# Kernel optimization log

Measured on AMD Instinct MI355X. Metric: run time of the kernel, lower is better.

## Reference

```python
import jax, jax.numpy as jnp
import numpy as np
import math

HIDDEN = 128

def setup_inputs() -> dict:
    key = jax.random.key(0)
    k1, k2, k3 = jax.random.split(key, 3)
    X = jax.random.normal(k1, (4, 4096, HIDDEN), dtype=jnp.float32)
    # nn.Linear(hidden, 3*hidden): weight [3H, H], bias [3H]
    bound = 1.0 / math.sqrt(HIDDEN)
    W = jax.random.uniform(k2, (3 * HIDDEN, HIDDEN), minval=-bound, maxval=bound, dtype=jnp.float32)
    b = jax.random.uniform(k3, (3 * HIDDEN,), minval=-bound, maxval=bound, dtype=jnp.float32)
    return {"X": X, "W": W, "b": b}

def reference(X, W, b):
    H = X.shape[-1]
    # fused QKV projection: X @ W^T + b -> [B, S, 3H]
    qkv = jnp.einsum('bsh,oh->bso', X, W) + b
    Q, K, V = jnp.split(qkv, 3, axis=-1)
    # scaled dot-product attention (single head)
    scores = jnp.einsum('bqh,bkh->bqk', Q, K) / jnp.sqrt(jnp.asarray(H, X.dtype))
    weights = jax.nn.softmax(scores, axis=-1)
    return jnp.einsum('bqk,bkh->bqh', weights, V)
```

## Files before the change

### kernel.cpp

```cpp
#include <hip/hip_runtime.h>
#include <hip/hip_fp16.h>

typedef _Float16 f16;
typedef __attribute__((ext_vector_type(8))) _Float16 f16x8;
typedef __attribute__((ext_vector_type(4))) float f32x4;
typedef __attribute__((ext_vector_type(4))) unsigned int u32x4;
typedef __attribute__((ext_vector_type(2))) unsigned int u32x2;

#define BB 4
#define SS 4096
#define HH 128
#define SC2 0.12752462157076558f
#define M2  5.7707801635558535f

union H2U { __half2 h; unsigned int u; };
union VU { u32x4 v; unsigned short s[8]; };
union F8U { u32x4 u; f16x8 h; };

__global__ __launch_bounds__(256) void wcvt(const float* __restrict__ W,
                                            f16* __restrict__ Wh)
{
    const int idx = (blockIdx.x * 256 + threadIdx.x) * 4;
    float4 v = *(const float4*)(W + idx);
    H2U h0, h1;
    h0.h = __floats2half2_rn(v.x, v.y);
    h1.h = __floats2half2_rn(v.z, v.w);
    u32x2 pk; pk.x = h0.u; pk.y = h1.u;
    *(u32x2*)(Wh + idx) = pk;
}

__global__ __launch_bounds__(256, 2) void qkv_gemm(
    const float* __restrict__ X, const f16* __restrict__ Wh,
    const float* __restrict__ bias, f16* __restrict__ Qh,
    f16* __restrict__ Kh, f16* __restrict__ Vh)
{
    const int bid = blockIdx.x;
    const int t = threadIdx.x;
    const int w = t >> 6, lane = t & 63;
    const int c = lane & 15, quad = lane >> 4;
    const int rbase = bid * 64;

    f16x8 wf[6][4];
#pragma unroll
    for (int mt = 0; mt < 6; ++mt) {
        const f16* wr = Wh + (size_t)(w * 96 + mt * 16 + c) * HH + quad * 8;
#pragma unroll
        for (int kc = 0; kc < 4; ++kc)
            wf[mt][kc] = *(const f16x8*)(wr + kc * 32);
    }
    float4 bb[6];
#pragma unroll
    for (int mt = 0; mt < 6; ++mt)
        bb[mt] = *(const float4*)&bias[w * 96 + mt * 16 + quad * 4];

#pragma unroll
    for (int nt = 0; nt < 4; ++nt) {
        f16x8 xf[4];
        const float* xr = X + (size_t)(rbase + nt * 16 + c) * HH + quad * 8;
#pragma unroll
        for (int kc = 0; kc < 4; ++kc) {
            float4 a = *(const float4*)(xr + kc * 32);
            float4 b = *(const float4*)(xr + kc * 32 + 4);
            H2U u0, u1, u2, u3;
            u0.h = __floats2half2_rn(a.x, a.y);
            u1.h = __floats2half2_rn(a.z, a.w);
            u2.h = __floats2half2_rn(b.x, b.y);
            u3.h = __floats2half2_rn(b.z, b.w);
            F8U pk; pk.u.x = u0.u; pk.u.y = u1.u; pk.u.z = u2.u; pk.u.w = u3.u;
            xf[kc] = pk.h;
        }
        f32x4 acc[6];
#pragma unroll
        for (int mt = 0; mt < 6; ++mt) acc[mt] = (f32x4)0.f;
#pragma unroll
        for (int kc = 0; kc < 4; ++kc)
#pragma unroll
            for (int mt = 0; mt < 6; ++mt)
                acc[mt] = __builtin_amdgcn_mfma_f32_16x16x32_f16(wf[mt][kc], xf[kc], acc[mt], 0, 0, 0);

        const int xrow = rbase + nt * 16 + c;
#pragma unroll
        for (int mt = 0; mt < 6; ++mt) {
            const int gcol = w * 96 + mt * 16;
            const int seg = gcol >> 7;
            const int cc = (gcol & 127) + quad * 4;
            f16* dst = (seg == 0) ? Qh : (seg == 1) ? Kh : Vh;
            H2U h0, h1;
            h0.h = __floats2half2_rn(acc[mt][0] + bb[mt].x, acc[mt][1] + bb[mt].y);
            h1.h = __floats2half2_rn(acc[mt][2] + bb[mt].z, acc[mt][3] + bb[mt].w);
            u32x2 pk; pk.x = h0.u; pk.y = h1.u;
            *(u32x2*)(dst + (size_t)xrow * HH + cc) = pk;
        }
    }
}

#define BM 128
#define BN 64
#define LK 136
#define LV 72
#define LP 40

__global__ __launch_bounds__(256, 2) void attn_mfma(
    const f16* __restrict__ Qh, const f16* __restrict__ Kh,
    const f16* __restrict__ Vh, float* __restrict__ out,
    float* __restrict__ Opart, float* __restrict__ l_arr, int nsplit)
{
    __shared__ f16 sK[BN * LK];
    __shared__ f16 sVt[HH * LV];
    __shared__ f16 sP[4][32 * LP];

    const int bid = blockIdx.x;
    const int split = bid >> 7;
    const int inner = bid & 127;
    const int batch = inner & 3;
    const int qtile = inner >> 2;
    const int t = threadIdx.x;
    const int w = t >> 6, lane = t & 63;
    const int c = lane & 15, quad = lane >> 4;

    const int s0 = (64 * split) / nsplit;
    const int s1 = (64 * (split + 1)) / nsplit;
    const int nst = s1 - s0;
    const int kstart = s0 * BN;

    const f16* Qb = Qh + (size_t)batch * SS * HH;
    const f16* Kb = Kh + (size_t)batch * SS * HH;
    const f16* Vb = Vh + (size_t)batch * SS * HH;
    const int qbase = qtile * BM + w * 32;

    f16x8 qf[2][4];
#pragma unroll
    for (int qt = 0; qt < 2; ++qt)
#pragma unroll
        for (int kc = 0; kc < 4; ++kc)
            qf[qt][kc] = *(const f16x8*)(Qb + (size_t)(qbase + qt * 16 + c) * HH + kc * 32 + quad * 8);

    const int kr = t >> 2, q4 = t & 3;
    const f16* kgp = Kb + (size_t)(kstart + kr) * HH + q4 * 32;
    f16* ksp = sK + kr * LK + q4 * 32;
    const int vkp = t & 31, vhq = t >> 5;
    const f16* vgp = Vb + (size_t)(kstart + 2 * vkp) * HH + vhq * 16;

    u32x4 kbuf[4], vb0[2], vb1[2];
#pragma unroll
    for (int i = 0; i < 4; ++i) kbuf[i] = *(const u32x4*)(kgp + i * 8);
#pragma unroll
    for (int i = 0; i < 2; ++i) {
        vb0[i] = *(const u32x4*)(vgp + i * 8);
        vb1[i] = *(const u32x4*)(vgp + HH + i * 8);
    }

    f32x4 oacc[2][8];
#pragma unroll
    for (int mt = 0; mt < 2; ++mt)
#pragma unroll
        for (int nt = 0; nt < 8; ++nt) oacc[mt][nt] = (f32x4)0.f;
    f32x4 oaccl[2];
    oaccl[0] = (f32x4)0.f; oaccl[1] = (f32x4)0.f;
    const f16x8 ones = {1, 1, 1, 1, 1, 1, 1, 1};

    for (int st = 0; st < nst; ++st) {
        __syncthreads();
#pragma unroll
        for (int i = 0; i < 4; ++i) *(u32x4*)(ksp + i * 8) = kbuf[i];
        {
            VU a0, a1, b0, b1;
            a0.v = vb0[0]; a1.v = vb0[1]; b0.v = vb1[0]; b1.v = vb1[1];
#pragma unroll
            for (int d = 0; d < 8; ++d) {
                unsigned int pk = (unsigned int)a0.s[d] | ((unsigned int)b0.s[d] << 16);
                *(unsigned int*)&sVt[(vhq * 16 + d) * LV + 2 * vkp] = pk;
            }
#pragma unroll
            for (int d = 0; d < 8; ++d) {
                unsigned int pk = (unsigned int)a1.s[d] | ((unsigned int)b1.s[d] << 16);
                *(unsigned int*)&sVt[(vhq * 16 + 8 + d) * LV + 2 * vkp] = pk;
            }
        }
        __syncthreads();
        if (st + 1 < nst) {
            const f16* kg = kgp + (size_t)(st + 1) * BN * HH;
#pragma unroll
            for (int i = 0; i < 4; ++i) kbuf[i] = *(const u32x4*)(kg + i * 8);
            const f16* vg = vgp + (size_t)(st + 1) * BN * HH;
#pragma unroll
            for (int i = 0; i < 2; ++i) {
                vb0[i] = *(const u32x4*)(vg + i * 8);
                vb1[i] = *(const u32x4*)(vg + HH + i * 8);
            }
        }

        f32x4 sacc[4][2];
#pragma unroll
        for (int km = 0; km < 4; ++km)
#pragma unroll
            for (int qt = 0; qt < 2; ++qt) sacc[km][qt] = (f32x4)0.f;
#pragma unroll
        for (int kc = 0; kc < 4; ++kc) {
#pragma unroll
            for (int km = 0; km < 4; ++km) {
                f16x8 kf = *(const f16x8*)&sK[(km * 16 + c) * LK + kc * 32 + quad * 8];
#pragma unroll
                for (int qt = 0; qt < 2; ++qt)
                    sacc[km][qt] = __builtin_amdgcn_mfma_f32_16x16x32_f16(kf, qf[qt][kc], sacc[km][qt], 0, 0, 0);
            }
        }

#pragma unroll
        for (int h = 0; h < 2; ++h) {
#pragma unroll
            for (int qt = 0; qt < 2; ++qt) {
#pragma unroll
                for (int km2 = 0; km2 < 2; ++km2) {
                    const int km = 2 * h + km2;
                    float p0 = exp2f(sacc[km][qt][0] * SC2 - M2);
                    float p1 = exp2f(sacc[km][qt][1] * SC2 - M2);
                    float p2 = exp2f(sacc[km][qt][2] * SC2 - M2);
                    float p3 = exp2f(sacc[km][qt][3] * SC2 - M2);
                    H2U u0, u1;
                    u0.h = __floats2half2_rn(p0, p1);
                    u1.h = __floats2half2_rn(p2, p3);
                    u32x2 pk; pk.x = u0.u; pk.y = u1.u;
                    *(u32x2*)&sP[w][(qt * 16 + c) * LP + km2 * 16 + quad * 4] = pk;
                }
            }
            f16x8 pf[2];
#pragma unroll
            for (int mt = 0; mt < 2; ++mt)
                pf[mt] = *(const f16x8*)&sP[w][(mt * 16 + c) * LP + quad * 8];
#pragma unroll
            for (int mt = 0; mt < 2; ++mt)
                oaccl[mt] = __builtin_amdgcn_mfma_f32_16x16x32_f16(pf[mt], ones, oaccl[mt], 0, 0, 0);
#pragma unroll
            for (int nt = 0; nt < 8; ++nt) {
                f16x8 vf = *(const f16x8*)&sVt[(nt * 16 + c) * LV + h * 32 + quad * 8];
#pragma unroll
                for (int mt = 0; mt < 2; ++mt)
                    oacc[mt][nt] = __builtin_amdgcn_mfma_f32_16x16x32_f16(pf[mt], vf, oacc[mt][nt], 0, 0, 0);
            }
        }
    }

    float* Ob = (split == 0) ? out : (Opart + (size_t)(split - 1) * BB * SS * HH);
    float* ob = Ob + (size_t)(batch * SS + qbase) * HH;
    if (nsplit == 1) {
#pragma unroll
        for (int mt = 0; mt < 2; ++mt) {
#pragma unroll
            for (int r = 0; r < 4; ++r) {
                const float lv = 1.f / oaccl[mt][r];
                const int row = mt * 16 + quad * 4 + r;
#pragma unroll
                for (int nt = 0; nt < 8; ++nt)
                    ob[(size_t)row * HH + nt * 16 + c] = oacc[mt][nt][r] * lv;
            }
        }
    } else {
#pragma unroll
        for (int mt = 0; mt < 2; ++mt) {
#pragma unroll
            for (int r = 0; r < 4; ++r) {
                const int row = mt * 16 + quad * 4 + r;
#pragma unroll
                for (int nt = 0; nt < 8; ++nt)
                    ob[(size_t)row * HH + nt * 16 + c] = oacc[mt][nt][r];
            }
        }
        if (c == 0) {
#pragma unroll
            for (int mt = 0; mt < 2; ++mt)
#pragma unroll
                for (int r = 0; r < 4; ++r)
                    l_arr[((size_t)split * BB + batch) * SS + qbase + mt * 16 + quad * 4 + r] = oaccl[mt][r];
        }
    }
}

__global__ __launch_bounds__(256) void attn_merge(
    float* __restrict__ out, const float* __restrict__ Opart,
    const float* __restrict__ l_arr, int nsplit)
{
    const int idx = blockIdx.x * 256 + threadIdx.x;
    const int chunk = idx & 31;
    const int q = (idx >> 5) & (SS - 1);
    const int b = idx >> 17;
    float L = 0.f;
    for (int s = 0; s < nsplit; ++s)
        L += l_arr[((size_t)s * BB + b) * SS + q];
    float4 a = *(const float4*)(out + ((size_t)b * SS + q) * HH + chunk * 4);
    for (int s = 1; s < nsplit; ++s) {
        const float* Op = Opart + (size_t)(s - 1) * BB * SS * HH;
        float4 o = *(const float4*)(Op + ((size_t)b * SS + q) * HH + chunk * 4);
        a.x += o.x; a.y += o.y; a.z += o.z; a.w += o.w;
    }
    const float inv = 1.f / L;
    a.x *= inv; a.y *= inv; a.z *= inv; a.w *= inv;
    *(float4*)(out + ((size_t)b * SS + q) * HH + chunk * 4) = a;
}

extern "C" void kernel_launch(void* const* d_in, const int* in_sizes, int n_in,
                              void* d_out, int out_size, void* d_ws, size_t ws_size,
                              hipStream_t stream) {
    const float* X = (const float*)d_in[0];
    const float* W = (const float*)d_in[1];
    const float* bias = (const float*)d_in[2];
    float* out = (float*)d_out;

    char* ws = (char*)d_ws;
    const size_t qkv_bytes = (size_t)3 * BB * SS * HH * sizeof(f16);
    const size_t wh_bytes  = (size_t)384 * HH * sizeof(f16);
    const size_t o_bytes   = (size_t)BB * SS * HH * sizeof(float);
    const size_t l_bytes   = (size_t)BB * SS * sizeof(float);

    int S = 1;
    for (int cand = 4; cand >= 2; --cand) {
        if (ws_size >= qkv_bytes + wh_bytes + (size_t)(cand - 1) * o_bytes + (size_t)cand * l_bytes) {
            S = cand; break;
        }
    }

    f16* Qh = (f16*)ws;
    f16* Kh = Qh + (size_t)BB * SS * HH;
    f16* Vh = Kh + (size_t)BB * SS * HH;
    f16* Wh = (f16*)(ws + qkv_bytes);
    float* Opart = (float*)(ws + qkv_bytes + wh_bytes);
    float* l_arr = (float*)(ws + qkv_bytes + wh_bytes + (size_t)(S - 1) * o_bytes);

    wcvt<<<48, 256, 0, stream>>>(W, Wh);
    qkv_gemm<<<256, 256, 0, stream>>>(X, Wh, bias, Qh, Kh, Vh);
    attn_mfma<<<128 * S, 256, 0, stream>>>(Qh, Kh, Vh, out, Opart, l_arr, S);
    if (S > 1)
        attn_merge<<<BB * SS * (HH / 4) / 256, 256, 0, stream>>>(out, Opart, l_arr, S);
}
```

Before: 128.5 us.

## Fuse split-K merge into attention via atomic last-block reduction; halve GEMM tile rows

The separate merge kernel is removed. Each split block now writes its partial output and its row sums to the workspace, then increments an atomic counter for its query tile, and the last-arriving block sums the partials, normalizes and writes the final output. This saves a kernel launch and a pass over the output, at the cost of a memset of the counters, extra workspace for split 0's partial, and fences. Separately, the QKV GEMM processes 32 rows per block instead of 64 and launches 512 blocks to improve occupancy and parallelism.

```diff
diff --git a/kernel.cpp b/kernel.cpp
--- a/kernel.cpp
+++ b/kernel.cpp
@@ -38,7 +38,7 @@
     const int t = threadIdx.x;
     const int w = t >> 6, lane = t & 63;
     const int c = lane & 15, quad = lane >> 4;
-    const int rbase = bid * 64;
+    const int rbase = bid * 32;
 
     f16x8 wf[6][4];
 #pragma unroll
@@ -54,7 +54,7 @@
         bb[mt] = *(const float4*)&bias[w * 96 + mt * 16 + quad * 4];
 
 #pragma unroll
-    for (int nt = 0; nt < 4; ++nt) {
+    for (int nt = 0; nt < 2; ++nt) {
         f16x8 xf[4];
         const float* xr = X + (size_t)(rbase + nt * 16 + c) * HH + quad * 8;
 #pragma unroll
@@ -103,11 +103,13 @@
 __global__ __launch_bounds__(256, 2) void attn_mfma(
     const f16* __restrict__ Qh, const f16* __restrict__ Kh,
     const f16* __restrict__ Vh, float* __restrict__ out,
-    float* __restrict__ Opart, float* __restrict__ l_arr, int nsplit)
+    float* __restrict__ Opart, float* __restrict__ l_arr,
+    int* __restrict__ ctr, int nsplit)
 {
     __shared__ f16 sK[BN * LK];
     __shared__ f16 sVt[HH * LV];
     __shared__ f16 sP[4][32 * LP];
+    __shared__ int rank_s;
 
     const int bid = blockIdx.x;
     const int split = bid >> 7;
@@ -241,9 +243,8 @@
         }
     }
 
-    float* Ob = (split == 0) ? out : (Opart + (size_t)(split - 1) * BB * SS * HH);
-    float* ob = Ob + (size_t)(batch * SS + qbase) * HH;
     if (nsplit == 1) {
+        float* ob = out + (size_t)(batch * SS + qbase) * HH;
 #pragma unroll
         for (int mt = 0; mt < 2; ++mt) {
 #pragma unroll
@@ -255,47 +256,55 @@
                     ob[(size_t)row * HH + nt * 16 + c] = oacc[mt][nt][r] * lv;
             }
         }
-    } else {
-#pragma unroll
-        for (int mt = 0; mt < 2; ++mt) {
-#pragma unroll
-            for (int r = 0; r < 4; ++r) {
-                const int row = mt * 16 + quad * 4 + r;
-#pragma unroll
-                for (int nt = 0; nt < 8; ++nt)
-                    ob[(size_t)row * HH + nt * 16 + c] = oacc[mt][nt][r];
-            }
-        }
-        if (c == 0) {
-#pragma unroll
-            for (int mt = 0; mt < 2; ++mt)
-#pragma unroll
-                for (int r = 0; r < 4; ++r)
-                    l_arr[((size_t)split * BB + batch) * SS + qbase + mt * 16 + quad * 4 + r] = oaccl[mt][r];
-        }
-    }
-}
-
-__global__ __launch_bounds__(256) void attn_merge(
-    float* __restrict__ out, const float* __restrict__ Opart,
-    const float* __restrict__ l_arr, int nsplit)
-{
-    const int idx = blockIdx.x * 256 + threadIdx.x;
-    const int chunk = idx & 31;
-    const int q = (idx >> 5) & (SS - 1);
-    const int b = idx >> 17;
-    float L = 0.f;
-    for (int s = 0; s < nsplit; ++s)
-        L += l_arr[((size_t)s * BB + b) * SS + q];
-    float4 a = *(const float4*)(out + ((size_t)b * SS + q) * HH + chunk * 4);
-    for (int s = 1; s < nsplit; ++s) {
-        const float* Op = Opart + (size_t)(s - 1) * BB * SS * HH;
-        float4 o = *(const float4*)(Op + ((size_t)b * SS + q) * HH + chunk * 4);
-        a.x += o.x; a.y += o.y; a.z += o.z; a.w += o.w;
-    }
-    const float inv = 1.f / L;
-    a.x *= inv; a.y *= inv; a.z *= inv; a.w *= inv;
-    *(float4*)(out + ((size_t)b * SS + q) * HH + chunk * 4) = a;
+        return;
+    }
+
+    float* ob = Opart + ((size_t)split * BB * SS + (size_t)batch * SS + qbase) * HH;
+#pragma unroll
+    for (int mt = 0; mt < 2; ++mt) {
+#pragma unroll
+        for (int r = 0; r < 4; ++r) {
+            const int row = mt * 16 + quad * 4 + r;
+#pragma unroll
+            for (int nt = 0; nt < 8; ++nt)
+                ob[(size_t)row * HH + nt * 16 + c] = oacc[mt][nt][r];
+        }
+    }
+    if (c == 0) {
+#pragma unroll
+        for (int mt = 0; mt < 2; ++mt)
+#pragma unroll
+            for (int r = 0; r < 4; ++r)
+                l_arr[((size_t)split * BB + batch) * SS + qbase + mt * 16 + quad * 4 + r] = oaccl[mt][r];
+    }
+
+    __threadfence();
+    if (t == 0)
+        rank_s = __hip_atomic_fetch_add(&ctr[inner], 1, __ATOMIC_ACQ_REL, __HIP_MEMORY_SCOPE_AGENT);
+    __syncthreads();
+    if (rank_s == nsplit - 1) {
+        __threadfence();
+        const int row = t >> 1;
+        const int ch0 = (t & 1) * 16;
+        const int q = qtile * BM + row;
+        float L = 0.f;
+        for (int s = 0; s < nsplit; ++s)
+            L += l_arr[((size_t)s * BB + batch) * SS + q];
+        const float inv = 1.f / L;
+        float* orow = out + ((size_t)batch * SS + q) * HH;
+        const size_t poff = ((size_t)batch * SS + q) * HH;
+        for (int i = 0; i < 16; ++i) {
+            const int col4 = ch0 + i;
+            float4 a = *(const float4*)(Opart + poff + col4 * 4);
+            for (int s = 1; s < nsplit; ++s) {
+                const float* Op = Opart + (size_t)s * BB * SS * HH + poff;
+                float4 o = *(const float4*)(Op + col4 * 4);
+                a.x += o.x; a.y += o.y; a.z += o.z; a.w += o.w;
+            }
+            a.x *= inv; a.y *= inv; a.z *= inv; a.w *= inv;
+            *(float4*)(orow + col4 * 4) = a;
+        }
+    }
 }
 
 extern "C" void kernel_launch(void* const* d_in, const int* in_sizes, int n_in,
@@ -311,10 +320,11 @@
     const size_t wh_bytes  = (size_t)384 * HH * sizeof(f16);
     const size_t o_bytes   = (size_t)BB * SS * HH * sizeof(float);
     const size_t l_bytes   = (size_t)BB * SS * sizeof(float);
+    const size_t ctr_bytes = 512;
 
     int S = 1;
     for (int cand = 4; cand >= 2; --cand) {
-        if (ws_size >= qkv_bytes + wh_bytes + (size_t)(cand - 1) * o_bytes + (size_t)cand * l_bytes) {
+        if (ws_size >= qkv_bytes + wh_bytes + (size_t)cand * (o_bytes + l_bytes) + ctr_bytes) {
             S = cand; break;
         }
     }
@@ -324,11 +334,11 @@
     f16* Vh = Kh + (size_t)BB * SS * HH;
     f16* Wh = (f16*)(ws + qkv_bytes);
     float* Opart = (float*)(ws + qkv_bytes + wh_bytes);
-    float* l_arr = (float*)(ws + qkv_bytes + wh_bytes + (size_t)(S - 1) * o_bytes);
-
+    float* l_arr = (float*)(ws + qkv_bytes + wh_bytes + (size_t)S * o_bytes);
+    int* ctr = (int*)(ws + qkv_bytes + wh_bytes + (size_t)S * (o_bytes + l_bytes));
+
+    if (S > 1) hipMemsetAsync(ctr, 0, ctr_bytes, stream);
     wcvt<<<48, 256, 0, stream>>>(W, Wh);
-    qkv_gemm<<<256, 256, 0, stream>>>(X, Wh, bias, Qh, Kh, Vh);
-    attn_mfma<<<128 * S, 256, 0, stream>>>(Qh, Kh, Vh, out, Opart, l_arr, S);
-    if (S > 1)
-        attn_merge<<<BB * SS * (HH / 4) / 256, 256, 0, stream>>>(out, Opart, l_arr, S);
+    qkv_gemm<<<512, 256, 0, stream>>>(X, Wh, bias, Qh, Kh, Vh);
+    attn_mfma<<<128 * S, 256, 0, stream>>>(Qh, Kh, Vh, out, Opart, l_arr, ctr, S);
 }
```

Result: slower. 228.2 us (+77.6%).
